# Kernel tuning notes

Hardware: AMD Instinct MI355X
Metric: run time of the kernel (lower is better)

Reference implementation:

```python
import jax, jax.numpy as jnp
import numpy as np

B = 16        # graphs per batch
N0 = 4096     # nodes per graph (equal-size graphs -> static TopK shapes)
DEG = 8       # avg degree
E = B * N0 * DEG
CW = 64
OUT = 256


def _seg_sum(vals, idx, n):
    return jax.ops.segment_sum(vals, idx, num_segments=n)


def _sage(x, src, dst, valid, wl, bl, wr, n):
    # PyG SAGEConv: lin_l(mean_{j->i} x_j) + lin_r(x_i); lin_r has no bias
    vf = valid.astype(x.dtype)
    msg = x[src] * vf[:, None]                     # [E, d]
    s = _seg_sum(msg, dst, n)
    cnt = _seg_sum(vf, dst, n)
    mean = s / jnp.maximum(cnt, 1.0)[:, None]
    return mean @ wl.T + bl + x @ wr.T


def _gcn(x, src, dst, valid, w, b, n):
    # PyG GCNConv: add self-loops, symmetric normalization
    h = x @ w.T
    vf = valid.astype(x.dtype)
    deg = 1.0 + _seg_sum(vf, dst, n)               # includes self-loop
    inv_sqrt = jax.lax.rsqrt(deg)
    norm = inv_sqrt[src] * inv_sqrt[dst] * vf      # [E]
    agg = _seg_sum(h[src] * norm[:, None], dst, n) + h * (1.0 / deg)[:, None]
    return agg + b


def _topk_pool(x, src, dst, valid, w, n_per_graph):
    # PyG TopKPooling: score = x@w/||w||, keep top ceil(ratio*n) per graph,
    # x' = x[perm] * tanh(score[perm]); reindex edges, drop edges with removed endpoints.
    k = (n_per_graph + 1) // 2
    score = (x @ w) / jnp.linalg.norm(w)
    vals, idx = jax.lax.top_k(score.reshape(B, n_per_graph), k)   # [B,k]
    offs = (jnp.arange(B, dtype=jnp.int32) * n_per_graph)[:, None]
    perm = (idx.astype(jnp.int32) + offs).reshape(-1)             # [B*k] global ids
    x_new = x[perm] * jnp.tanh(vals.reshape(-1))[:, None]
    new_idx = jnp.full((B * n_per_graph,), -1, dtype=jnp.int32).at[perm].set(
        jnp.arange(B * k, dtype=jnp.int32))
    s2, d2 = new_idx[src], new_idx[dst]
    valid2 = valid & (s2 >= 0) & (d2 >= 0)
    s2 = jnp.where(valid2, s2, 0)
    d2 = jnp.where(valid2, d2, 0)
    return x_new, s2, d2, valid2, k


def _readout(x, k):
    xg = x.reshape(B, k, -1)
    return jnp.concatenate([xg.max(axis=1), xg.mean(axis=1)], axis=1)  # [B, 2d]


def _forward(x, edge_src, edge_dst, w1_l, b1, w1_r, w2_l, b2, w2_r, w3_l, b3, w3_r,
             w4, b4, w5, b5, w6, b6, p1, p2, p3, p4, p5, p6,
             lw1, lb1, lw2, lb2, lw3, lb3):
    src, dst = edge_src, edge_dst
    valid = jnp.ones((E,), dtype=bool)
    n = N0
    sage_ps = [(w1_l, b1, w1_r), (w2_l, b2, w2_r), (w3_l, b3, w3_r)]
    gcn_ps = [(w4, b4), (w5, b5), (w6, b6)]
    pools = [p1, p2, p3, p4, p5, p6]
    h = x
    z = None
    for i in range(6):
        if i < 3:
            wl, bl, wr = sage_ps[i]
            h = jax.nn.relu(_sage(h, src, dst, valid, wl, bl, wr, B * n))
        else:
            w, b = gcn_ps[i - 3]
            h = jax.nn.relu(_gcn(h, src, dst, valid, w, b, B * n))
        h, src, dst, valid, n = _topk_pool(h, src, dst, valid, pools[i], n)
        r = _readout(h, n)
        z = r if z is None else z + r
    z = jax.nn.relu(z @ lw1.T + lb1)
    z = jax.nn.relu(z @ lw2.T + lb2)
    z = z @ lw3.T + lb3
    return jax.nn.softmax(z, axis=1)


def setup_inputs() -> dict:
    key = jax.random.key(0)
    ks = jax.random.split(key, 40)

    def nrm(k, shape, s=0.1):
        return jax.random.normal(k, shape, dtype=jnp.float32) * s

    # per-graph random edges (both endpoints inside the same graph block)
    epg = N0 * DEG
    src_l = jax.random.randint(ks[0], (B, epg), 0, N0, dtype=jnp.int32)
    dst_l = jax.random.randint(ks[1], (B, epg), 0, N0, dtype=jnp.int32)
    offs = (jnp.arange(B, dtype=jnp.int32) * N0)[:, None]
    inp = {
        'x': jax.random.normal(ks[2], (B * N0, 2), dtype=jnp.float32),
        'edge_src': (src_l + offs).reshape(-1),
        'edge_dst': (dst_l + offs).reshape(-1),
        'w1_l': nrm(ks[3], (CW, 2)), 'b1': nrm(ks[4], (CW,)), 'w1_r': nrm(ks[5], (CW, 2)),
        'w2_l': nrm(ks[6], (CW, CW)), 'b2': nrm(ks[7], (CW,)), 'w2_r': nrm(ks[8], (CW, CW)),
        'w3_l': nrm(ks[9], (CW, CW)), 'b3': nrm(ks[10], (CW,)), 'w3_r': nrm(ks[11], (CW, CW)),
        'w4': nrm(ks[12], (CW, CW)), 'b4': jnp.zeros((CW,), jnp.float32),
        'w5': nrm(ks[13], (CW, CW)), 'b5': jnp.zeros((CW,), jnp.float32),
        'w6': nrm(ks[14], (CW, CW)), 'b6': jnp.zeros((CW,), jnp.float32),
        'p1': nrm(ks[15], (CW,)), 'p2': nrm(ks[16], (CW,)), 'p3': nrm(ks[17], (CW,)),
        'p4': nrm(ks[18], (CW,)), 'p5': nrm(ks[19], (CW,)), 'p6': nrm(ks[20], (CW,)),
        'lw1': nrm(ks[21], (128, 2 * CW)), 'lb1': nrm(ks[22], (128,)),
        'lw2': nrm(ks[23], (64, 128)), 'lb2': nrm(ks[24], (64,)),
        'lw3': nrm(ks[25], (OUT, 64)), 'lb3': nrm(ks[26], (OUT,)),
    }
    return inp


def reference(x, edge_src, edge_dst, w1_l, b1, w1_r, w2_l, b2, w2_r, w3_l, b3, w3_r,
              w4, b4, w5, b5, w6, b6, p1, p2, p3, p4, p5, p6,
              lw1, lb1, lw2, lb2, lw3, lb3):
    return _forward(x, edge_src, edge_dst, w1_l, b1, w1_r, w2_l, b2, w2_r,
                    w3_l, b3, w3_r, w4, b4, w5, b5, w6, b6,
                    p1, p2, p3, p4, p5, p6, lw1, lb1, lw2, lb2, lw3, lb3)
```

## Files before the change

### kernel.cpp

```cpp
#include <hip/hip_runtime.h>
#include <math.h>

#define NB 16
#define N0 4096
#define NE 524288


static __global__ void k_count(const int* __restrict__ dst, int* __restrict__ cnt) {
  int e = blockIdx.x * 256 + threadIdx.x;
  if (e >= NE) return;
  atomicAdd(&cnt[dst[e]], 1);
}

static __global__ void k_fill0(const int* __restrict__ src, const int* __restrict__ dst,
                               int* __restrict__ cursor, int* __restrict__ list) {
  int e = blockIdx.x * 256 + threadIdx.x;
  if (e >= NE) return;
  int d = dst[e];
  int slot = atomicAdd(&cursor[d], 1);
  list[slot] = src[e];
}


static __global__ void k_scan1(const int* __restrict__ in, int* __restrict__ out,
                               int* __restrict__ bsum, int n) {
  __shared__ int ts[256];
  int base = blockIdx.x * 1024 + threadIdx.x * 4;
  int a0 = (base + 0 < n) ? in[base + 0] : 0;
  int a1 = (base + 1 < n) ? in[base + 1] : 0;
  int a2 = (base + 2 < n) ? in[base + 2] : 0;
  int a3 = (base + 3 < n) ? in[base + 3] : 0;
  int s = a0 + a1 + a2 + a3;
  ts[threadIdx.x] = s;
  __syncthreads();
  for (int off = 1; off < 256; off <<= 1) {
    int v = (threadIdx.x >= off) ? ts[threadIdx.x - off] : 0;
    __syncthreads();
    ts[threadIdx.x] += v;
    __syncthreads();
  }
  int excl = ts[threadIdx.x] - s;
  if (base + 0 < n) out[base + 0] = excl;
  excl += a0;
  if (base + 1 < n) out[base + 1] = excl;
  excl += a1;
  if (base + 2 < n) out[base + 2] = excl;
  excl += a2;
  if (base + 3 < n) out[base + 3] = excl;
  if (threadIdx.x == 255) bsum[blockIdx.x] = ts[255];
}

static __global__ void k_scan2(int* __restrict__ bsum, int nb) {
  __shared__ int t[64];
  int i = threadIdx.x;
  int v = (i < nb) ? bsum[i] : 0;
  t[i] = v;
  __syncthreads();
  for (int off = 1; off < 64; off <<= 1) {
    int u = (i >= off) ? t[i - off] : 0;
    __syncthreads();
    t[i] += u;
    __syncthreads();
  }
  if (i < nb) bsum[i] = t[i] - v;
}

static __global__ void k_scan3(int* __restrict__ out, int* __restrict__ out2,
                               const int* __restrict__ bsum, int n) {
  int i = blockIdx.x * 256 + threadIdx.x;
  if (i < n) {
    int v = out[i] + bsum[i >> 10];
    out[i] = v;
    if (out2) out2[i] = v;
  }
}


static __global__ void k_newcount(const int* __restrict__ perm, const int* __restrict__ offs,
                                  const int* __restrict__ cnt, const int* __restrict__ list,
                                  const int* __restrict__ newidx, int* __restrict__ ncnt,
                                  int newn) {
  int nn = blockIdx.x * 256 + threadIdx.x;
  if (nn >= newn) return;
  int old = perm[nn];
  int st = offs[old], c = cnt[old];
  int cc = 0;
  for (int j = 0; j < c; ++j) cc += (newidx[list[st + j]] >= 0);
  ncnt[nn] = cc;
}

static __global__ void k_newfill(const int* __restrict__ perm, const int* __restrict__ offs,
                                 const int* __restrict__ cnt, const int* __restrict__ list,
                                 const int* __restrict__ newidx, const int* __restrict__ noffs,
                                 int* __restrict__ nlist, int newn) {
  int nn = blockIdx.x * 256 + threadIdx.x;
  if (nn >= newn) return;
  int old = perm[nn];
  int st = offs[old], c = cnt[old];
  int pos = noffs[nn];
  for (int j = 0; j < c; ++j) {
    int s2 = newidx[list[st + j]];
    if (s2 >= 0) nlist[pos++] = s2;
  }
}


static __global__ void k_pnorm(const float* __restrict__ p0, const float* __restrict__ p1,
                               const float* __restrict__ p2, const float* __restrict__ p3,
                               const float* __restrict__ p4, const float* __restrict__ p5,
                               float* __restrict__ pnbuf) {
  const float* pp = p0;
  switch (blockIdx.x) {
    case 1: pp = p1; break;
    case 2: pp = p2; break;
    case 3: pp = p3; break;
    case 4: pp = p4; break;
    case 5: pp = p5; break;
    default: break;
  }
  double v = (double)pp[threadIdx.x];
  v *= v;
#pragma unroll
  for (int off = 1; off < 64; off <<= 1) v += __shfl_xor(v, off);
  if (threadIdx.x == 0) pnbuf[blockIdx.x] = (float)(1.0 / sqrt(v));
}


static __global__ void k_sage_gather2(const float* __restrict__ x, const int* __restrict__ offs,
                                      const int* __restrict__ cnt, const int* __restrict__ list,
                                      float* __restrict__ mean, int ntot) {
  int v = blockIdx.x * 256 + threadIdx.x;
  if (v >= ntot) return;
  int st = offs[v], c = cnt[v];
  float s0 = 0.f, s1 = 0.f;
  for (int j = 0; j < c; ++j) {
    int s = list[st + j];
    s0 += x[s * 2 + 0];
    s1 += x[s * 2 + 1];
  }
  float inv = 1.0f / fmaxf((float)c, 1.0f);
  mean[v * 2 + 0] = s0 * inv;
  mean[v * 2 + 1] = s1 * inv;
}

static __global__ void k_sage0(const float* __restrict__ x, const float* __restrict__ mean,
                               const float* __restrict__ wl, const float* __restrict__ blv,
                               const float* __restrict__ wr, const float* __restrict__ pvec,
                               const float* __restrict__ pnbuf, float* __restrict__ h,
                               float* __restrict__ score, int ntot) {
  __shared__ float wlT[2][65], wrT[2][65];
  if (threadIdx.x < 128) {
    int o = threadIdx.x >> 1, d = threadIdx.x & 1;
    wlT[d][o] = wl[o * 2 + d];
    wrT[d][o] = wr[o * 2 + d];
  }
  __syncthreads();
  int o = threadIdx.x & 63, vl = threadIdx.x >> 6;
  int base = blockIdx.x * 16 + vl * 4;
  float pn = pnbuf[0];
  float psl = pvec[o];
#pragma unroll
  for (int r = 0; r < 4; ++r) {
    int v = base + r;
    if (v >= ntot) break;
    float acc = blv[o] + mean[v * 2 + 0] * wlT[0][o] + mean[v * 2 + 1] * wlT[1][o] +
                x[v * 2 + 0] * wrT[0][o] + x[v * 2 + 1] * wrT[1][o];
    float hval = fmaxf(acc, 0.0f);
    h[(size_t)v * 64 + o] = hval;
    double sc = (double)hval * (double)psl;
#pragma unroll
    for (int off = 1; off < 64; off <<= 1) sc += __shfl_xor(sc, off);
    if (o == 0) score[v] = (float)sc * pn;
  }
}

static __global__ __launch_bounds__(256) void k_sage_mm(
    const float* __restrict__ x, const int* __restrict__ offs, const int* __restrict__ cnt,
    const int* __restrict__ list, const float* __restrict__ wl, const float* __restrict__ blv,
    const float* __restrict__ wr, const float* __restrict__ pvec,
    const float* __restrict__ pnbuf, int pidx, float* __restrict__ h,
    float* __restrict__ score) {
  __shared__ float smem[16384];
  __shared__ float psh[64], bsh[64];
  float* xT = smem;
  float* mT = smem + 4096;
  float* wlT = smem + 8192;
  float* wrT = smem + 12288;
  int t = threadIdx.x;
  size_t nb = blockIdx.x;

  const float4* wl4 = (const float4*)wl;
  const float4* wr4 = (const float4*)wr;
  for (int i4 = t; i4 < 1024; i4 += 256) {
    int o = i4 >> 4, db = (i4 & 15) << 2;
    float4 L = wl4[i4], R = wr4[i4];
    float Lv[4] = {L.x, L.y, L.z, L.w}, Rv[4] = {R.x, R.y, R.z, R.w};
    int og = o >> 2, o3 = o & 3;
#pragma unroll
    for (int j = 0; j < 4; ++j) {
      int d = db + j;
      int col = ((og ^ (d & 15)) << 2) | o3;
      wlT[(d << 6) + col] = Lv[j];
      wrT[(d << 6) + col] = Rv[j];
    }
  }
  if (t < 64) {
    psh[t] = pvec[t];
    bsh[t] = blv[t];
  }
  const float4* x4 = (const float4*)(x + nb * 4096);
  for (int i = t; i < 1024; i += 256) {
    int node = i >> 4, db = (i & 15) << 2;
    float4 a = x4[i];
    float av[4] = {a.x, a.y, a.z, a.w};
    int ng = node >> 2, n0 = node & 3;
#pragma unroll
    for (int j = 0; j < 4; ++j) {
      int d = db + j;
      xT[(d << 6) + (((ng ^ (d & 15)) << 2) | n0)] = av[j];
    }
  }
  {
    int lane = t & 63, w = t >> 6;
    int stq[16], cq[16];
    float accq[16];
    int cmax = 0;
#pragma unroll
    for (int q = 0; q < 16; ++q) {
      int gv = (int)nb * 64 + w * 16 + q;
      stq[q] = offs[gv];
      cq[q] = cnt[gv];
      accq[q] = 0.f;
      cmax = max(cmax, cq[q]);
    }
    for (int j = 0; j < cmax; ++j) {
#pragma unroll
      for (int q = 0; q < 16; ++q) {
        if (j < cq[q]) accq[q] += x[(size_t)list[stq[q] + j] * 64 + lane];
      }
    }
#pragma unroll
    for (int q = 0; q < 16; ++q) {
      int node = w * 16 + q;
      float mval = accq[q] * (1.0f / fmaxf((float)cq[q], 1.0f));
      int col = (((node >> 2) ^ (lane & 15)) << 2) | (node & 3);
      mT[(lane << 6) + col] = mval;
    }
  }
  __syncthreads();

  int tx = t & 15, ty = t >> 4;
  float acc[4][4] = {};
#pragma unroll 4
  for (int k = 0; k < 64; ++k) {
    int s = k & 15;
    int ca = (tx ^ s) << 2, cb = (ty ^ s) << 2;
    const float4 a = *(const float4*)&xT[(k << 6) + ca];
    const float4 m = *(const float4*)&mT[(k << 6) + ca];
    const float4 L = *(const float4*)&wlT[(k << 6) + cb];
    const float4 R = *(const float4*)&wrT[(k << 6) + cb];
    float A[4] = {a.x, a.y, a.z, a.w}, M[4] = {m.x, m.y, m.z, m.w};
    float Lv[4] = {L.x, L.y, L.z, L.w}, Rv[4] = {R.x, R.y, R.z, R.w};
#pragma unroll
    for (int r = 0; r < 4; ++r)
#pragma unroll
      for (int c = 0; c < 4; ++c) acc[r][c] += M[r] * Lv[c] + A[r] * Rv[c];
  }

  float pn = pnbuf[pidx];
  float hv[4][4];
  double sp[4];
#pragma unroll
  for (int r = 0; r < 4; ++r) {
    sp[r] = 0.0;
#pragma unroll
    for (int c = 0; c < 4; ++c) {
      float v = fmaxf(acc[r][c] + bsh[(ty << 2) + c], 0.0f);
      hv[r][c] = v;
      sp[r] += (double)v * (double)psh[(ty << 2) + c];
    }
  }
  __syncthreads();
  float* hT = smem;
  double* sred = (double*)(smem + 8192);
#pragma unroll
  for (int r = 0; r < 4; ++r) {
    int node = (tx << 2) + r;
    int nk = node & 15;
#pragma unroll
    for (int c = 0; c < 4; ++c) hT[node * 68 + (((ty ^ nk) << 2) | c)] = hv[r][c];
    sred[(ty << 6) + node] = sp[r];
  }
  __syncthreads();
  float4* h4 = (float4*)(h + nb * 4096);
  for (int i = t; i < 1024; i += 256) {
    int node = i >> 4, q = i & 15;
    h4[i] = *(const float4*)&hT[node * 68 + ((q ^ (node & 15)) << 2)];
  }
  if (t < 64) {
    double ssum = 0.0;
    for (int g = 0; g < 16; ++g) ssum += sred[(g << 6) + t];
    score[nb * 64 + t] = (float)ssum * pn;
  }
}


static __global__ __launch_bounds__(256) void k_gcn_mm(const float* __restrict__ x,
                                                       const float* __restrict__ w,
                                                       float* __restrict__ h1) {
  __shared__ float smem[8192];
  float* xT = smem;
  float* wT = smem + 4096;
  int t = threadIdx.x;
  size_t nb = blockIdx.x;
  const float4* w4 = (const float4*)w;
  for (int i4 = t; i4 < 1024; i4 += 256) {
    int o = i4 >> 4, db = (i4 & 15) << 2;
    float4 W = w4[i4];
    float Wv[4] = {W.x, W.y, W.z, W.w};
    int og = o >> 2, o3 = o & 3;
#pragma unroll
    for (int j = 0; j < 4; ++j) {
      int d = db + j;
      wT[(d << 6) + (((og ^ (d & 15)) << 2) | o3)] = Wv[j];
    }
  }
  const float4* x4 = (const float4*)(x + nb * 4096);
  for (int i = t; i < 1024; i += 256) {
    int node = i >> 4, db = (i & 15) << 2;
    float4 a = x4[i];
    float av[4] = {a.x, a.y, a.z, a.w};
    int ng = node >> 2, n0 = node & 3;
#pragma unroll
    for (int j = 0; j < 4; ++j) {
      int d = db + j;
      xT[(d << 6) + (((ng ^ (d & 15)) << 2) | n0)] = av[j];
    }
  }
  __syncthreads();
  int tx = t & 15, ty = t >> 4;
  float acc[4][4] = {};
#pragma unroll 4
  for (int k = 0; k < 64; ++k) {
    int s = k & 15;
    const float4 a = *(const float4*)&xT[(k << 6) + ((tx ^ s) << 2)];
    const float4 W = *(const float4*)&wT[(k << 6) + ((ty ^ s) << 2)];
    float A[4] = {a.x, a.y, a.z, a.w}, Wv[4] = {W.x, W.y, W.z, W.w};
#pragma unroll
    for (int r = 0; r < 4; ++r)
#pragma unroll
      for (int c = 0; c < 4; ++c) acc[r][c] += A[r] * Wv[c];
  }
  __syncthreads();
  float* hT = smem;
#pragma unroll
  for (int r = 0; r < 4; ++r) {
    int node = (tx << 2) + r;
    int nk = node & 15;
#pragma unroll
    for (int c = 0; c < 4; ++c) hT[node * 68 + (((ty ^ nk) << 2) | c)] = acc[r][c];
  }
  __syncthreads();
  float4* h4 = (float4*)(h1 + nb * 4096);
  for (int i = t; i < 1024; i += 256) {
    int node = i >> 4, q = i & 15;
    h4[i] = *(const float4*)&hT[node * 68 + ((q ^ (node & 15)) << 2)];
  }
}

static __global__ void k_gcn_gather(const float* __restrict__ h1, const int* __restrict__ offs,
                                    const int* __restrict__ cnt, const int* __restrict__ list,
                                    const float* __restrict__ b, const float* __restrict__ pvec,
                                    const float* __restrict__ pnbuf, int pidx,
                                    float* __restrict__ h, float* __restrict__ score, int ntot) {
  int lane = threadIdx.x & 63, vl = threadIdx.x >> 6;
  int v = blockIdx.x * 4 + vl;
  if (v >= ntot) return;
  int st = offs[v], c = cnt[v];
  float degv = 1.0f + (float)c;
  float ivd = 1.0f / sqrtf(degv);
  float acc = 0.f;
  for (int j = 0; j < c; ++j) {
    int s = list[st + j];
    float nrm = (1.0f / sqrtf(1.0f + (float)cnt[s])) * ivd;
    acc += h1[(size_t)s * 64 + lane] * nrm;
  }
  float outv = fmaxf(acc + h1[(size_t)v * 64 + lane] * (1.0f / degv) + b[lane], 0.0f);
  h[(size_t)v * 64 + lane] = outv;
  double sc = (double)outv * (double)pvec[lane];
#pragma unroll
  for (int off = 1; off < 64; off <<= 1) sc += __shfl_xor(sc, off);
  if (lane == 0) score[v] = (float)sc * pnbuf[pidx];
}


static __global__ void k_chunksort(const float* __restrict__ score,
                                   unsigned long long* __restrict__ runs, int n_per, int k,
                                   int* __restrict__ newidx, int* __restrict__ perm, int single) {
  extern __shared__ unsigned long long sk[];
  int CH = blockDim.x;
  int g0 = blockIdx.x * CH;
  int b = g0 / n_per;
  int i = threadIdx.x;
  int gi = g0 + i;
  int li = gi - b * n_per;
  unsigned u = __float_as_uint(score[gi]);
  unsigned s = (u & 0x80000000u) ? u : ~(u | 0x80000000u);
  sk[i] = ((unsigned long long)s << 32) | (unsigned)li;
  __syncthreads();
  for (int ksz = 2; ksz <= CH; ksz <<= 1) {
    for (int j = ksz >> 1; j > 0; j >>= 1) {
      int ixj = i ^ j;
      if (ixj > i) {
        unsigned long long a = sk[i], c = sk[ixj];
        bool up = ((i & ksz) == 0);
        if ((a > c) == up) {
          sk[i] = c;
          sk[ixj] = a;
        }
      }
      __syncthreads();
    }
  }
  if (!single) {
    runs[gi] = sk[i];
  } else {
    int r = i;
    int idx = (int)(sk[r] & 0xFFFFFFFFu);
    int gidx = b * n_per + idx;
    if (r < k) {
      perm[b * k + r] = gidx;
      newidx[gidx] = b * k + r;
    } else {
      newidx[gidx] = -1;
    }
  }
}

static __global__ void k_merge(const unsigned long long* __restrict__ in,
                               unsigned long long* __restrict__ out, int L, int ntot, int n_per,
                               int k, int* __restrict__ newidx, int* __restrict__ perm,
                               int final) {
  int g = blockIdx.x * 256 + threadIdx.x;
  if (g >= ntot) return;
  unsigned long long key = in[g];
  int pair = g / (2 * L);
  int base = pair * 2 * L;
  int t = g - base;
  const unsigned long long* sib;
  int p;
  if (t < L) {
    sib = in + base + L;
    p = t;
  } else {
    sib = in + base;
    p = t - L;
  }
  int lo = 0, hi = L;
  while (lo < hi) {
    int mid = (lo + hi) >> 1;
    lo = (sib[mid] < key) ? mid + 1 : lo;
    hi = (sib[mid] < key) ? hi : mid;
  }
  int pos = p + lo;
  if (!final) {
    out[base + pos] = key;
  } else {
    int b = base / n_per;
    int idx = (int)(key & 0xFFFFFFFFu);
    int gidx = b * n_per + idx;
    if (pos < k) {
      perm[b * k + pos] = gidx;
      newidx[gidx] = b * k + pos;
    } else {
      newidx[gidx] = -1;
    }
  }
}


static __global__ __launch_bounds__(1024) void k_gather_ro(
    const float* __restrict__ h, const float* __restrict__ score, const int* __restrict__ perm,
    float* __restrict__ xnew, float* __restrict__ pmax, float* __restrict__ psum) {
  __shared__ float tile[64 * 68];
  __shared__ float pm[16][65], ps[16][65];
  int t = threadIdx.x;
  int node = t >> 4, q = t & 15;
  int nn = blockIdx.x * 64 + node;
  int old = perm[nn];
  float tm = tanhf(score[old]);
  float4 v = *(const float4*)&h[(size_t)old * 64 + q * 4];
  v.x *= tm;
  v.y *= tm;
  v.z *= tm;
  v.w *= tm;
  *(float4*)&xnew[(size_t)nn * 64 + q * 4] = v;
  *(float4*)&tile[node * 68 + ((q ^ (node & 15)) << 2)] = v;
  __syncthreads();
  int slot = t >> 6, d = t & 63;
  int q2 = d >> 2, i3 = d & 3;
  float m = -INFINITY, s = 0.f;
#pragma unroll
  for (int r = 0; r < 4; ++r) {
    int nd = slot * 4 + r;
    float val = tile[nd * 68 + (((q2 ^ (nd & 15)) << 2) | i3)];
    m = fmaxf(m, val);
    s += val;
  }
  pm[slot][d] = m;
  ps[slot][d] = s;
  __syncthreads();
  if (t < 64) {
    float mm = -INFINITY, ss = 0.f;
#pragma unroll
    for (int sl = 0; sl < 16; ++sl) {
      mm = fmaxf(mm, pm[sl][t]);
      ss += ps[sl][t];
    }
    pmax[(size_t)blockIdx.x * 64 + t] = mm;
    psum[(size_t)blockIdx.x * 64 + t] = ss;
  }
}

static __global__ void k_readout_comb(const float* __restrict__ pmax,
                                      const float* __restrict__ psum, float* __restrict__ z,
                                      int k, int nch) {
  int b = blockIdx.x, d = threadIdx.x;
  float m = -INFINITY, s = 0.0f;
  for (int c = 0; c < nch; ++c) {
    m = fmaxf(m, pmax[((size_t)b * nch + c) * 64 + d]);
    s += psum[((size_t)b * nch + c) * 64 + d];
  }
  z[b * 128 + d] += m;
  z[b * 128 + 64 + d] += s / (float)k;
}


static __global__ void k_mlp(const float* __restrict__ z, const float* __restrict__ lw1,
                             const float* __restrict__ lb1, const float* __restrict__ lw2,
                             const float* __restrict__ lb2, const float* __restrict__ lw3,
                             const float* __restrict__ lb3, float* __restrict__ out) {
  __shared__ float zs[128], t1[128], t2[64], t3[256], red[256];
  int b = blockIdx.x, tid = threadIdx.x;
  if (tid < 128) zs[tid] = z[b * 128 + tid];
  __syncthreads();
  if (tid < 128) {
    double a = 0.0;
    for (int d = 0; d < 128; ++d) a += (double)lw1[tid * 128 + d] * (double)zs[d];
    t1[tid] = fmaxf((float)a + lb1[tid], 0.0f);
  }
  __syncthreads();
  if (tid < 64) {
    double a = 0.0;
    for (int d = 0; d < 128; ++d) a += (double)lw2[tid * 128 + d] * (double)t1[d];
    t2[tid] = fmaxf((float)a + lb2[tid], 0.0f);
  }
  __syncthreads();
  {
    double a = 0.0;
    for (int d = 0; d < 64; ++d) a += (double)lw3[tid * 64 + d] * (double)t2[d];
    t3[tid] = (float)a + lb3[tid];
  }
  __syncthreads();
  red[tid] = t3[tid];
  __syncthreads();
  for (int s = 128; s > 0; s >>= 1) {
    if (tid < s) red[tid] = fmaxf(red[tid], red[tid + s]);
    __syncthreads();
  }
  float mx = red[0];
  __syncthreads();
  float e = expf(t3[tid] - mx);
  red[tid] = e;
  __syncthreads();
  for (int s = 128; s > 0; s >>= 1) {
    if (tid < s) red[tid] += red[tid + s];
    __syncthreads();
  }
  out[b * 256 + tid] = e / red[0];
}


extern "C" void kernel_launch(void* const* d_in, const int* in_sizes, int n_in,
                              void* d_out, int out_size, void* d_ws, size_t ws_size,
                              hipStream_t stream) {
  const float* x0 = (const float*)d_in[0];
  const int* esrc0 = (const int*)d_in[1];
  const int* edst0 = (const int*)d_in[2];
  const float* WL[3] = {(const float*)d_in[3], (const float*)d_in[6], (const float*)d_in[9]};
  const float* BL[3] = {(const float*)d_in[4], (const float*)d_in[7], (const float*)d_in[10]};
  const float* WR[3] = {(const float*)d_in[5], (const float*)d_in[8], (const float*)d_in[11]};
  const float* WG[3] = {(const float*)d_in[12], (const float*)d_in[14], (const float*)d_in[16]};
  const float* BG[3] = {(const float*)d_in[13], (const float*)d_in[15], (const float*)d_in[17]};
  const float* P[6] = {(const float*)d_in[18], (const float*)d_in[19], (const float*)d_in[20],
                       (const float*)d_in[21], (const float*)d_in[22], (const float*)d_in[23]};
  const float* lw1 = (const float*)d_in[24];
  const float* lb1 = (const float*)d_in[25];
  const float* lw2 = (const float*)d_in[26];
  const float* lb2 = (const float*)d_in[27];
  const float* lw3 = (const float*)d_in[28];
  const float* lb3 = (const float*)d_in[29];

  char* ws = (char*)d_ws;
  size_t off = 0;
  auto alloc = [&](size_t bytes) -> void* {
    void* p = ws + off;
    off += (bytes + 255) & ~(size_t)255;
    return p;
  };
  float* hA = (float*)alloc((size_t)65536 * 64 * 4);
  float* hB = (float*)alloc((size_t)32768 * 64 * 4);
  float* mean = (float*)alloc((size_t)65536 * 2 * 4);
  float* tmp = (float*)alloc((size_t)8192 * 64 * 4);
  float* score = (float*)alloc((size_t)65536 * 4);
  int* newidx = (int*)alloc((size_t)65536 * 4);
  int* perm = (int*)alloc((size_t)32768 * 4);
  int* cntA = (int*)alloc((size_t)65536 * 4);
  int* cntB = (int*)alloc((size_t)65536 * 4);
  int* offsA = (int*)alloc((size_t)65536 * 4);
  int* offsB = (int*)alloc((size_t)65536 * 4);
  int* cursor = (int*)alloc((size_t)65536 * 4);
  int* bsum = (int*)alloc((size_t)64 * 4);
  int* listA = (int*)alloc((size_t)NE * 4);
  int* listB = (int*)alloc((size_t)NE * 4);
  float* z = (float*)alloc((size_t)16 * 128 * 4);
  float* pmax = (float*)alloc((size_t)NB * 32 * 64 * 4);
  float* psum = (float*)alloc((size_t)NB * 32 * 64 * 4);
  unsigned long long* keyA = (unsigned long long*)alloc((size_t)65536 * 8);
  unsigned long long* keyB = (unsigned long long*)alloc((size_t)65536 * 8);
  float* pnbuf = (float*)alloc((size_t)64 * 4);
  if (off > ws_size) return;

  auto scan = [&](int* cntp, int* offsp, int* curp, int n) {
    int nblk = (n + 1023) / 1024;
    k_scan1<<<nblk, 256, 0, stream>>>(cntp, offsp, bsum, n);
    k_scan2<<<1, 64, 0, stream>>>(bsum, nblk);
    k_scan3<<<(n + 255) / 256, 256, 0, stream>>>(offsp, curp, bsum, n);
  };

  hipMemsetAsync(z, 0, 16 * 128 * 4, stream);
  k_pnorm<<<6, 64, 0, stream>>>(P[0], P[1], P[2], P[3], P[4], P[5], pnbuf);

  hipMemsetAsync(cntA, 0, (size_t)65536 * 4, stream);
  k_count<<<NE / 256, 256, 0, stream>>>(edst0, cntA);
  scan(cntA, offsA, cursor, 65536);
  k_fill0<<<NE / 256, 256, 0, stream>>>(esrc0, edst0, cursor, listA);

  const float* xcur = x0;
  int* ccnt = cntA;
  int* coffs = offsA;
  int* clist = listA;

  for (int i = 0; i < 6; ++i) {
    int n_per = N0 >> i;
    int ntot = NB * n_per;
    int k = n_per >> 1;

    if (i == 0) {
      k_sage_gather2<<<(ntot + 255) / 256, 256, 0, stream>>>(xcur, coffs, ccnt, clist, mean, ntot);
      k_sage0<<<(ntot + 15) / 16, 256, 0, stream>>>(xcur, mean, WL[0], BL[0], WR[0], P[0], pnbuf,
                                                    hA, score, ntot);
    } else if (i < 3) {
      k_sage_mm<<<ntot / 64, 256, 0, stream>>>(xcur, coffs, ccnt, clist, WL[i], BL[i], WR[i],
                                               P[i], pnbuf, i, hA, score);
    } else {
      int g = i - 3;
      k_gcn_mm<<<ntot / 64, 256, 0, stream>>>(xcur, WG[g], tmp);
      k_gcn_gather<<<(ntot + 3) / 4, 256, 0, stream>>>(tmp, coffs, ccnt, clist, BG[g], P[i],
                                                       pnbuf, i, hA, score, ntot);
    }

    int CH = (n_per < 1024) ? n_per : 1024;
    int single = (CH == n_per) ? 1 : 0;
    k_chunksort<<<ntot / CH, CH, (size_t)CH * 8, stream>>>(score, keyA, n_per, k, newidx, perm,
                                                           single);
    if (!single) {
      unsigned long long* cur = keyA;
      unsigned long long* nxt = keyB;
      for (int L = CH; L * 2 <= n_per; L <<= 1) {
        int fin = (L * 2 == n_per) ? 1 : 0;
        k_merge<<<(ntot + 255) / 256, 256, 0, stream>>>(cur, nxt, L, ntot, n_per, k, newidx, perm,
                                                        fin);
        unsigned long long* t2 = cur;
        cur = nxt;
        nxt = t2;
      }
    }

    int nch = k / 64;
    k_gather_ro<<<NB * nch, 1024, 0, stream>>>(hA, score, perm, hB, pmax, psum);

    if (i < 5) {
      int newn = NB * k;
      int* ncnt = (i & 1) ? cntA : cntB;
      int* noffs = (i & 1) ? offsA : offsB;
      int* nlist = (i & 1) ? listA : listB;
      k_newcount<<<(newn + 255) / 256, 256, 0, stream>>>(perm, coffs, ccnt, clist, newidx, ncnt,
                                                         newn);
      scan(ncnt, noffs, nullptr, newn);
      k_newfill<<<(newn + 255) / 256, 256, 0, stream>>>(perm, coffs, ccnt, clist, newidx, noffs,
                                                        nlist, newn);
      ccnt = ncnt;
      coffs = noffs;
      clist = nlist;
    }

    k_readout_comb<<<NB, 64, 0, stream>>>(pmax, psum, z, k, nch);
    xcur = hB;
  }

  k_mlp<<<NB, 256, 0, stream>>>(z, lw1, lb1, lw2, lb2, lw3, lb3, (float*)d_out);
}
```

Baseline: 410.2 us.

## Pretranspose weights once and stage per-block edge lists in LDS

Adds a prep kernel that writes swizzled, transposed copies of the sage and GCN weights into workspace once per call. The per-block weight transpose into shared memory in the matmul kernels is removed, and the matmul now reads the pre-swizzled weights directly from global memory. The sage_mm kernel also copies the block's contiguous neighbor-list slice into LDS, up to a capacity, before gathering. Shared memory use per block drops, which may allow more blocks per CU. The cost is that the inner matmul loop now reads weights from global memory and cache instead of LDS.

New measurement: 407.4 us. No clear change (-0.7%).

```diff
diff --git a/kernel.cpp b/kernel.cpp
--- a/kernel.cpp
+++ b/kernel.cpp
@@ -4,6 +4,7 @@
 #define NB 16
 #define N0 4096
 #define NE 524288
+#define CAPE 1280
 
 
 static __global__ void k_count(const int* __restrict__ dst, int* __restrict__ cnt) {
@@ -125,6 +126,35 @@
   if (threadIdx.x == 0) pnbuf[blockIdx.x] = (float)(1.0 / sqrt(v));
 }
 
+static __global__ void k_wprep(const float* __restrict__ w0, const float* __restrict__ w1,
+                               const float* __restrict__ w2, const float* __restrict__ w3,
+                               const float* __restrict__ w4, const float* __restrict__ w5,
+                               const float* __restrict__ w6, float* __restrict__ wp) {
+  const float* src = w0;
+  switch (blockIdx.x) {
+    case 1: src = w1; break;
+    case 2: src = w2; break;
+    case 3: src = w3; break;
+    case 4: src = w4; break;
+    case 5: src = w5; break;
+    case 6: src = w6; break;
+    default: break;
+  }
+  float* dst = wp + (size_t)blockIdx.x * 4096;
+  const float4* w4p = (const float4*)src;
+  for (int i4 = threadIdx.x; i4 < 1024; i4 += 256) {
+    int o = i4 >> 4, db = (i4 & 15) << 2;
+    float4 W = w4p[i4];
+    float Wv[4] = {W.x, W.y, W.z, W.w};
+    int og = o >> 2, o3 = o & 3;
+#pragma unroll
+    for (int j = 0; j < 4; ++j) {
+      int d = db + j;
+      dst[(d << 6) + (((og ^ (d & 15)) << 2) | o3)] = Wv[j];
+    }
+  }
+}
+
 
 static __global__ void k_sage_gather2(const float* __restrict__ x, const int* __restrict__ offs,
                                       const int* __restrict__ cnt, const int* __restrict__ list,
@@ -176,34 +206,18 @@
 
 static __global__ __launch_bounds__(256) void k_sage_mm(
     const float* __restrict__ x, const int* __restrict__ offs, const int* __restrict__ cnt,
-    const int* __restrict__ list, const float* __restrict__ wl, const float* __restrict__ blv,
-    const float* __restrict__ wr, const float* __restrict__ pvec,
+    const int* __restrict__ list, const float* __restrict__ wlT, const float* __restrict__ blv,
+    const float* __restrict__ wrT, const float* __restrict__ pvec,
     const float* __restrict__ pnbuf, int pidx, float* __restrict__ h,
     float* __restrict__ score) {
-  __shared__ float smem[16384];
+  __shared__ float smem[8192];
   __shared__ float psh[64], bsh[64];
+  __shared__ int lds_list[CAPE];
   float* xT = smem;
   float* mT = smem + 4096;
-  float* wlT = smem + 8192;
-  float* wrT = smem + 12288;
   int t = threadIdx.x;
   size_t nb = blockIdx.x;
 
-  const float4* wl4 = (const float4*)wl;
-  const float4* wr4 = (const float4*)wr;
-  for (int i4 = t; i4 < 1024; i4 += 256) {
-    int o = i4 >> 4, db = (i4 & 15) << 2;
-    float4 L = wl4[i4], R = wr4[i4];
-    float Lv[4] = {L.x, L.y, L.z, L.w}, Rv[4] = {R.x, R.y, R.z, R.w};
-    int og = o >> 2, o3 = o & 3;
-#pragma unroll
-    for (int j = 0; j < 4; ++j) {
-      int d = db + j;
-      int col = ((og ^ (d & 15)) << 2) | o3;
-      wlT[(d << 6) + col] = Lv[j];
-      wrT[(d << 6) + col] = Rv[j];
-    }
-  }
   if (t < 64) {
     psh[t] = pvec[t];
     bsh[t] = blv[t];
@@ -220,6 +234,13 @@
       xT[(d << 6) + (((ng ^ (d & 15)) << 2) | n0)] = av[j];
     }
   }
+  int gv0 = (int)nb * 64;
+  int st0 = offs[gv0];
+  int nedge = offs[gv0 + 63] + cnt[gv0 + 63] - st0;
+  int ncap = (nedge < CAPE) ? nedge : CAPE;
+  for (int e = t; e < ncap; e += 256) lds_list[e] = list[st0 + e];
+  __syncthreads();
+
   {
     int lane = t & 63, w = t >> 6;
     int stq[16], cq[16];
@@ -227,8 +248,8 @@
     int cmax = 0;
 #pragma unroll
     for (int q = 0; q < 16; ++q) {
-      int gv = (int)nb * 64 + w * 16 + q;
-      stq[q] = offs[gv];
+      int gv = gv0 + w * 16 + q;
+      stq[q] = offs[gv] - st0;
       cq[q] = cnt[gv];
       accq[q] = 0.f;
       cmax = max(cmax, cq[q]);
@@ -236,7 +257,11 @@
     for (int j = 0; j < cmax; ++j) {
 #pragma unroll
       for (int q = 0; q < 16; ++q) {
-        if (j < cq[q]) accq[q] += x[(size_t)list[stq[q] + j] * 64 + lane];
+        if (j < cq[q]) {
+          int idx = stq[q] + j;
+          int sn = (idx < ncap) ? lds_list[idx] : list[st0 + idx];
+          accq[q] += x[(size_t)sn * 64 + lane];
+        }
       }
     }
 #pragma unroll
@@ -282,7 +307,7 @@
   }
   __syncthreads();
   float* hT = smem;
-  double* sred = (double*)(smem + 8192);
+  double* sred = (double*)(smem + 4608);
 #pragma unroll
   for (int r = 0; r < 4; ++r) {
     int node = (tx << 2) + r;
@@ -306,25 +331,12 @@
 
 
 static __global__ __launch_bounds__(256) void k_gcn_mm(const float* __restrict__ x,
-                                                       const float* __restrict__ w,
+                                                       const float* __restrict__ wT,
                                                        float* __restrict__ h1) {
-  __shared__ float smem[8192];
+  __shared__ float smem[4608];
   float* xT = smem;
-  float* wT = smem + 4096;
   int t = threadIdx.x;
   size_t nb = blockIdx.x;
-  const float4* w4 = (const float4*)w;
-  for (int i4 = t; i4 < 1024; i4 += 256) {
-    int o = i4 >> 4, db = (i4 & 15) << 2;
-    float4 W = w4[i4];
-    float Wv[4] = {W.x, W.y, W.z, W.w};
-    int og = o >> 2, o3 = o & 3;
-#pragma unroll
-    for (int j = 0; j < 4; ++j) {
-      int d = db + j;
-      wT[(d << 6) + (((og ^ (d & 15)) << 2) | o3)] = Wv[j];
-    }
-  }
   const float4* x4 = (const float4*)(x + nb * 4096);
   for (int i = t; i < 1024; i += 256) {
     int node = i >> 4, db = (i & 15) << 2;
@@ -629,6 +641,7 @@
   unsigned long long* keyA = (unsigned long long*)alloc((size_t)65536 * 8);
   unsigned long long* keyB = (unsigned long long*)alloc((size_t)65536 * 8);
   float* pnbuf = (float*)alloc((size_t)64 * 4);
+  float* wp = (float*)alloc((size_t)7 * 4096 * 4);
   if (off > ws_size) return;
 
   auto scan = [&](int* cntp, int* offsp, int* curp, int n) {
@@ -640,6 +653,7 @@
 
   hipMemsetAsync(z, 0, 16 * 128 * 4, stream);
   k_pnorm<<<6, 64, 0, stream>>>(P[0], P[1], P[2], P[3], P[4], P[5], pnbuf);
+  k_wprep<<<7, 256, 0, stream>>>(WL[1], WR[1], WL[2], WR[2], WG[0], WG[1], WG[2], wp);
 
   hipMemsetAsync(cntA, 0, (size_t)65536 * 4, stream);
   k_count<<<NE / 256, 256, 0, stream>>>(edst0, cntA);
@@ -661,11 +675,13 @@
       k_sage0<<<(ntot + 15) / 16, 256, 0, stream>>>(xcur, mean, WL[0], BL[0], WR[0], P[0], pnbuf,
                                                     hA, score, ntot);
     } else if (i < 3) {
-      k_sage_mm<<<ntot / 64, 256, 0, stream>>>(xcur, coffs, ccnt, clist, WL[i], BL[i], WR[i],
-                                               P[i], pnbuf, i, hA, score);
+      const float* wlp = wp + (size_t)((i - 1) * 2 + 0) * 4096;
+      const float* wrp = wp + (size_t)((i - 1) * 2 + 1) * 4096;
+      k_sage_mm<<<ntot / 64, 256, 0, stream>>>(xcur, coffs, ccnt, clist, wlp, BL[i], wrp, P[i],
+                                               pnbuf, i, hA, score);
     } else {
       int g = i - 3;
-      k_gcn_mm<<<ntot / 64, 256, 0, stream>>>(xcur, WG[g], tmp);
+      k_gcn_mm<<<ntot / 64, 256, 0, stream>>>(xcur, wp + (size_t)(4 + g) * 4096, tmp);
       k_gcn_gather<<<(ntot + 3) / 4, 256, 0, stream>>>(tmp, coffs, ccnt, clist, BG[g], P[i],
                                                        pnbuf, i, hA, score, ntot);
     }
```
